# Kernel tuning notes

Measured on AMD Instinct MI355X. Metric: run time of the kernel, lower is better.

## Reference

```python
import jax, jax.numpy as jnp
import numpy as np

DIM = 96
HEADS = 3
HEAD_DIM = DIM // HEADS
WIN = (4, 4, 4)
N_WIN = WIN[0] * WIN[1] * WIN[2]  # 64 tokens per window
HIDDEN = int(DIM * 4.0)
EPS = 1e-5


def setup_inputs() -> dict:
    key = jax.random.key(0)
    ks = jax.random.split(key, 16)
    s = lambda fan: 1.0 / np.sqrt(fan)
    return {
        "x": jax.random.normal(ks[0], (1, 64, 96, 96, 96), jnp.float32),
        "g1": jnp.ones((DIM,), jnp.float32),
        "b1": jnp.zeros((DIM,), jnp.float32),
        "wq": jax.random.normal(ks[1], (DIM, DIM), jnp.float32) * s(DIM),
        "bq": jnp.zeros((DIM,), jnp.float32),
        "wkv": jax.random.normal(ks[2], (DIM, 2 * DIM), jnp.float32) * s(DIM),
        "bkv": jnp.zeros((2 * DIM,), jnp.float32),
        "wp": jax.random.normal(ks[3], (DIM, DIM), jnp.float32) * s(DIM),
        "bp": jnp.zeros((DIM,), jnp.float32),
        "g2": jnp.ones((DIM,), jnp.float32),
        "b2": jnp.zeros((DIM,), jnp.float32),
        "w1": jax.random.normal(ks[4], (DIM, HIDDEN), jnp.float32) * s(DIM),
        "bm1": jnp.zeros((HIDDEN,), jnp.float32),
        "w2": jax.random.normal(ks[5], (HIDDEN, DIM), jnp.float32) * s(HIDDEN),
        "bm2": jnp.zeros((DIM,), jnp.float32),
    }


def _layernorm(x, g, b):
    mu = jnp.mean(x, axis=-1, keepdims=True)
    var = jnp.mean(jnp.square(x - mu), axis=-1, keepdims=True)
    return (x - mu) * jax.lax.rsqrt(var + EPS) * g + b


def _window_partition(x):
    B, D, H, W, C = x.shape
    wd, wh, ww = WIN
    x = x.reshape(B, D // wd, wd, H // wh, wh, W // ww, ww, C)
    x = x.transpose(0, 1, 3, 5, 2, 4, 6, 7)
    return x.reshape(-1, N_WIN, C)


def _window_reverse(win, B, D, H, W):
    wd, wh, ww = WIN
    C = win.shape[-1]
    x = win.reshape(B, D // wd, H // wh, W // ww, wd, wh, ww, C)
    x = x.transpose(0, 1, 4, 2, 5, 3, 6, 7)
    return x.reshape(B, D, H, W, C)


def reference(x, g1, b1, wq, bq, wkv, bkv, wp, bp, g2, b2, w1, bm1, w2, bm2):
    B, D, H, W, C = x.shape
    # --- part 1: LN -> window attention -> residual ---
    h = _layernorm(x, g1, b1)
    # D,H,W chosen divisible by window size, so padding is a no-op
    xw = _window_partition(h)                       # (nW, N, C)
    nW = xw.shape[0]
    q = (xw @ wq + bq).reshape(nW, N_WIN, HEADS, HEAD_DIM)
    kv = (xw @ wkv + bkv).reshape(nW, N_WIN, 2, HEADS, HEAD_DIM)
    k, v = kv[:, :, 0], kv[:, :, 1]                 # (nW, N, h, hd)
    scale = HEAD_DIM ** -0.5
    attn = jnp.einsum("wnhd,wmhd->whnm", q * scale, k)
    attn = jax.nn.softmax(attn, axis=-1)
    out = jnp.einsum("whnm,wmhd->wnhd", attn, v).reshape(nW, N_WIN, C)
    out = out @ wp + bp
    attn_out = _window_reverse(out, B, D, H, W)
    x = x + attn_out
    # --- part 2: LN -> MLP -> residual ---
    h2 = _layernorm(x, g2, b2)
    h2 = jax.nn.gelu(h2 @ w1 + bm1, approximate=False) @ w2 + bm2
    return x + h2
```

## Files before the change

### kernel.cpp

```cpp
#include <hip/hip_runtime.h>

typedef __bf16 bf16x8 __attribute__((ext_vector_type(8)));
typedef __bf16 bf16x4 __attribute__((ext_vector_type(4)));
typedef float f32x4 __attribute__((ext_vector_type(4)));

#define MFMA(a,b,c) __builtin_amdgcn_mfma_f32_16x16x32_bf16(a, b, c, 0, 0, 0)

__device__ __forceinline__ float gelu_f(float t) {
    float t2 = t * t;
    float m = t * __builtin_fmaf(-0.07135481627f, t2, -1.5957691216f);
    float e = __expf(m);
    return t * __builtin_amdgcn_rcpf(1.0f + e);
}

__global__ void prep_weights(const float* __restrict__ wq, const float* __restrict__ wkv,
                             const float* __restrict__ wp, const float* __restrict__ w1,
                             const float* __restrict__ w2, __bf16* __restrict__ ws) {
    int i = blockIdx.x * 256 + threadIdx.x;
    const float scale = 0.17677669529663687f;
    if (i < 9216) {
        int n = i / 96, k = i % 96;
        ws[i] = (__bf16)(wq[k * 96 + n] * scale);
    } else if (i < 27648) {
        int j = i - 9216; int n = j / 96, k = j % 96;
        ws[i] = (__bf16)(wkv[k * 192 + n]);
    } else if (i < 36864) {
        int j = i - 27648; int n = j / 96, k = j % 96;
        ws[i] = (__bf16)(wp[k * 96 + n]);
    } else if (i < 73728) {
        int j = i - 36864; int n = j / 96, k = j % 96;
        ws[i] = (__bf16)(w1[k * 384 + n]);
    } else if (i < 110592) {
        int j = i - 73728; int n = j / 384, k = j % 384;
        ws[i] = (__bf16)(w2[k * 96 + n]);
    }
}

#define LDH 104

__global__ __launch_bounds__(256, 2) void attn_kernel(
    const float* __restrict__ x, const float* __restrict__ g1v, const float* __restrict__ b1v,
    const float* __restrict__ bq, const float* __restrict__ bkv, const float* __restrict__ bp,
    const __bf16* __restrict__ ws, float* __restrict__ xmid)
{
    const __bf16* wqt  = ws;
    const __bf16* wkvt = ws + 9216;
    const __bf16* wpt  = ws + 27648;

    __shared__ __align__(16) __bf16 h_lds[64 * LDH];
    __shared__ __align__(16) __bf16 q_lds[64 * LDH];
    __shared__ __align__(16) __bf16 k_lds[64 * LDH];
    __shared__ __align__(16) __bf16 vt_lds[96 * 72];
    __shared__ __align__(16) __bf16 p_lds[4 * 16 * 72];

    const int tid = threadIdx.x;
    const int wv = tid >> 6, lane = tid & 63;
    const int c = lane & 15, g = lane >> 4;
    const int mp = wv >> 1, ng = wv & 1;

    const int wid = blockIdx.x;
    const int wdI = wid / 576, rem = wid % 576, whI = rem / 24, wwI = rem % 24;
    const int tok = tid >> 2, cseg = (tid & 3) * 24;
    const int dz = tok >> 4, hy = (tok >> 2) & 3, wx = tok & 3;
    const long gbase = (((long)(wdI * 4 + dz) * 96 + (whI * 4 + hy)) * 96 + (wwI * 4 + wx)) * 96 + cseg;

    float xr[24];
    #pragma unroll
    for (int j = 0; j < 6; ++j) {
        float4 v = *reinterpret_cast<const float4*>(x + gbase + j * 4);
        xr[j*4+0] = v.x; xr[j*4+1] = v.y; xr[j*4+2] = v.z; xr[j*4+3] = v.w;
    }
    float s = 0.f;
    #pragma unroll
    for (int j = 0; j < 24; ++j) s += xr[j];
    s += __shfl_xor(s, 1); s += __shfl_xor(s, 2);
    float mu = s * (1.0f / 96.0f);
    float vs = 0.f;
    #pragma unroll
    for (int j = 0; j < 24; ++j) { float d = xr[j] - mu; vs += d * d; }
    vs += __shfl_xor(vs, 1); vs += __shfl_xor(vs, 2);
    float rstd = rsqrtf(vs * (1.0f / 96.0f) + 1e-5f);
    #pragma unroll
    for (int j = 0; j < 6; ++j) {
        float4 gv = *reinterpret_cast<const float4*>(g1v + cseg + j * 4);
        float4 bv = *reinterpret_cast<const float4*>(b1v + cseg + j * 4);
        h_lds[tok * LDH + cseg + j*4+0] = (__bf16)((xr[j*4+0] - mu) * rstd * gv.x + bv.x);
        h_lds[tok * LDH + cseg + j*4+1] = (__bf16)((xr[j*4+1] - mu) * rstd * gv.y + bv.y);
        h_lds[tok * LDH + cseg + j*4+2] = (__bf16)((xr[j*4+2] - mu) * rstd * gv.z + bv.z);
        h_lds[tok * LDH + cseg + j*4+3] = (__bf16)((xr[j*4+3] - mu) * rstd * gv.w + bv.w);
    }
    __syncthreads();

    {
        f32x4 acc[2][3];
        #pragma unroll
        for (int mi = 0; mi < 2; ++mi)
            #pragma unroll
            for (int nl = 0; nl < 3; ++nl) acc[mi][nl] = (f32x4){0.f, 0.f, 0.f, 0.f};
        #pragma unroll
        for (int kc = 0; kc < 3; ++kc) {
            bf16x8 a[2];
            #pragma unroll
            for (int mi = 0; mi < 2; ++mi)
                a[mi] = *reinterpret_cast<const bf16x8*>(&h_lds[((mp*2+mi)*16 + c) * LDH + kc*32 + g*8]);
            #pragma unroll
            for (int nl = 0; nl < 3; ++nl) {
                int nt = ng * 3 + nl;
                bf16x8 b = *reinterpret_cast<const bf16x8*>(&wqt[(nt*16 + c) * 96 + kc*32 + g*8]);
                #pragma unroll
                for (int mi = 0; mi < 2; ++mi)
                    acc[mi][nl] = MFMA(a[mi], b, acc[mi][nl]);
            }
        }
        #pragma unroll
        for (int nl = 0; nl < 3; ++nl) {
            int n = (ng * 3 + nl) * 16 + c;
            float bias = bq[n] * 0.17677669529663687f;
            #pragma unroll
            for (int mi = 0; mi < 2; ++mi)
                #pragma unroll
                for (int r = 0; r < 4; ++r)
                    q_lds[((mp*2+mi)*16 + g*4 + r) * LDH + n] = (__bf16)(acc[mi][nl][r] + bias);
        }
    }

    {
        f32x4 acc[4][3];
        #pragma unroll
        for (int m = 0; m < 4; ++m)
            #pragma unroll
            for (int nl = 0; nl < 3; ++nl) acc[m][nl] = (f32x4){0.f, 0.f, 0.f, 0.f};
        #pragma unroll
        for (int kc = 0; kc < 3; ++kc) {
            bf16x8 a[4];
            #pragma unroll
            for (int m = 0; m < 4; ++m)
                a[m] = *reinterpret_cast<const bf16x8*>(&h_lds[(m*16 + c) * LDH + kc*32 + g*8]);
            #pragma unroll
            for (int nl = 0; nl < 3; ++nl) {
                int nt = wv * 3 + nl;
                bf16x8 b = *reinterpret_cast<const bf16x8*>(&wkvt[(nt*16 + c) * 96 + kc*32 + g*8]);
                #pragma unroll
                for (int m = 0; m < 4; ++m)
                    acc[m][nl] = MFMA(a[m], b, acc[m][nl]);
            }
        }
        #pragma unroll
        for (int nl = 0; nl < 3; ++nl) {
            int n = (wv * 3 + nl) * 16 + c;
            float bias = bkv[n];
            if (wv < 2) {
                #pragma unroll
                for (int m = 0; m < 4; ++m)
                    #pragma unroll
                    for (int r = 0; r < 4; ++r)
                        k_lds[(m*16 + g*4 + r) * LDH + n] = (__bf16)(acc[m][nl][r] + bias);
            } else {
                int nv = n - 96;
                #pragma unroll
                for (int m = 0; m < 4; ++m) {
                    bf16x4 pk;
                    pk.x = (__bf16)(acc[m][nl][0] + bias);
                    pk.y = (__bf16)(acc[m][nl][1] + bias);
                    pk.z = (__bf16)(acc[m][nl][2] + bias);
                    pk.w = (__bf16)(acc[m][nl][3] + bias);
                    *reinterpret_cast<bf16x4*>(&vt_lds[nv * 72 + m*16 + g*4]) = pk;
                }
            }
        }
    }
    __syncthreads();

    __bf16* p_w = &p_lds[wv * (16 * 72)];
    #pragma unroll
    for (int h = 0; h < 3; ++h) {
        f32x4 sacc[4];
        #pragma unroll
        for (int nt = 0; nt < 4; ++nt) sacc[nt] = (f32x4){0.f, 0.f, 0.f, 0.f};
        bf16x8 a = *reinterpret_cast<const bf16x8*>(&q_lds[(wv*16 + c) * LDH + h*32 + g*8]);
        #pragma unroll
        for (int nt = 0; nt < 4; ++nt) {
            bf16x8 b = *reinterpret_cast<const bf16x8*>(&k_lds[(nt*16 + c) * LDH + h*32 + g*8]);
            sacc[nt] = MFMA(a, b, sacc[nt]);
        }
        float mx[4];
        #pragma unroll
        for (int r = 0; r < 4; ++r) {
            float m0 = fmaxf(fmaxf(sacc[0][r], sacc[1][r]), fmaxf(sacc[2][r], sacc[3][r]));
            m0 = fmaxf(m0, __shfl_xor(m0, 1));
            m0 = fmaxf(m0, __shfl_xor(m0, 2));
            m0 = fmaxf(m0, __shfl_xor(m0, 4));
            m0 = fmaxf(m0, __shfl_xor(m0, 8));
            mx[r] = m0;
        }
        float p[4][4];
        #pragma unroll
        for (int nt = 0; nt < 4; ++nt)
            #pragma unroll
            for (int r = 0; r < 4; ++r)
                p[nt][r] = __expf(sacc[nt][r] - mx[r]);
        float rsinv[4];
        #pragma unroll
        for (int r = 0; r < 4; ++r) {
            float s0 = p[0][r] + p[1][r] + p[2][r] + p[3][r];
            s0 += __shfl_xor(s0, 1); s0 += __shfl_xor(s0, 2);
            s0 += __shfl_xor(s0, 4); s0 += __shfl_xor(s0, 8);
            rsinv[r] = __builtin_amdgcn_rcpf(s0);
        }
        #pragma unroll
        for (int nt = 0; nt < 4; ++nt)
            #pragma unroll
            for (int r = 0; r < 4; ++r)
                p_w[(g*4 + r) * 72 + nt*16 + c] = (__bf16)p[nt][r];

        f32x4 oacc[2];
        oacc[0] = (f32x4){0.f, 0.f, 0.f, 0.f};
        oacc[1] = (f32x4){0.f, 0.f, 0.f, 0.f};
        #pragma unroll
        for (int kc = 0; kc < 2; ++kc) {
            bf16x8 pa = *reinterpret_cast<const bf16x8*>(&p_w[c * 72 + kc*32 + g*8]);
            #pragma unroll
            for (int n2 = 0; n2 < 2; ++n2) {
                bf16x8 b = *reinterpret_cast<const bf16x8*>(&vt_lds[(h*32 + n2*16 + c) * 72 + kc*32 + g*8]);
                oacc[n2] = MFMA(pa, b, oacc[n2]);
            }
        }
        #pragma unroll
        for (int n2 = 0; n2 < 2; ++n2)
            #pragma unroll
            for (int r = 0; r < 4; ++r)
                h_lds[(wv*16 + g*4 + r) * LDH + h*32 + n2*16 + c] = (__bf16)(oacc[n2][r] * rsinv[r]);
    }
    __syncthreads();

    {
        f32x4 acc[2][3];
        #pragma unroll
        for (int mi = 0; mi < 2; ++mi)
            #pragma unroll
            for (int nl = 0; nl < 3; ++nl) acc[mi][nl] = (f32x4){0.f, 0.f, 0.f, 0.f};
        #pragma unroll
        for (int kc = 0; kc < 3; ++kc) {
            bf16x8 a[2];
            #pragma unroll
            for (int mi = 0; mi < 2; ++mi)
                a[mi] = *reinterpret_cast<const bf16x8*>(&h_lds[((mp*2+mi)*16 + c) * LDH + kc*32 + g*8]);
            #pragma unroll
            for (int nl = 0; nl < 3; ++nl) {
                int nt = ng * 3 + nl;
                bf16x8 b = *reinterpret_cast<const bf16x8*>(&wpt[(nt*16 + c) * 96 + kc*32 + g*8]);
                #pragma unroll
                for (int mi = 0; mi < 2; ++mi)
                    acc[mi][nl] = MFMA(a[mi], b, acc[mi][nl]);
            }
        }
        __syncthreads();
        #pragma unroll
        for (int nl = 0; nl < 3; ++nl) {
            int n = (ng * 3 + nl) * 16 + c;
            float bias = bp[n];
            #pragma unroll
            for (int mi = 0; mi < 2; ++mi)
                #pragma unroll
                for (int r = 0; r < 4; ++r)
                    q_lds[((mp*2+mi)*16 + g*4 + r) * LDH + n] = (__bf16)(acc[mi][nl][r] + bias);
        }
    }
    __syncthreads();

    #pragma unroll
    for (int j = 0; j < 6; ++j) {
        float4 v;
        v.x = xr[j*4+0] + (float)q_lds[tok * LDH + cseg + j*4+0];
        v.y = xr[j*4+1] + (float)q_lds[tok * LDH + cseg + j*4+1];
        v.z = xr[j*4+2] + (float)q_lds[tok * LDH + cseg + j*4+2];
        v.w = xr[j*4+3] + (float)q_lds[tok * LDH + cseg + j*4+3];
        *reinterpret_cast<float4*>(xmid + gbase + j * 4) = v;
    }
}

#define LDU 104
#define LDC2 104

__global__ __launch_bounds__(384, 3) void mlp_kernel(
    float* __restrict__ xio, const float* __restrict__ g2v, const float* __restrict__ b2v,
    const float* __restrict__ bm1, const float* __restrict__ bm2,
    const __bf16* __restrict__ ws)
{
    const __bf16* w1t = ws + 36864;
    const __bf16* w2t = ws + 73728;

    __shared__ __align__(16) __bf16 u_lds[64 * LDU];
    __shared__ __align__(16) __bf16 hid[64 * LDC2];

    const int tid = threadIdx.x;
    const int wv = tid >> 6, lane = tid & 63;
    const int c = lane & 15, g = lane >> 4;

    const int tok = tid >> 2, cseg = (tid & 3) * 24;
    const long gaddr = ((long)blockIdx.x * 64 + tok) * 96 + cseg;

    const f32x4 fzero = {0.f, 0.f, 0.f, 0.f};

    if (tid < 256) {
        float xr[24];
        #pragma unroll
        for (int j = 0; j < 6; ++j) {
            float4 v = *reinterpret_cast<const float4*>(xio + gaddr + j * 4);
            xr[j*4+0] = v.x; xr[j*4+1] = v.y; xr[j*4+2] = v.z; xr[j*4+3] = v.w;
        }
        float s = 0.f;
        #pragma unroll
        for (int j = 0; j < 24; ++j) s += xr[j];
        s += __shfl_xor(s, 1); s += __shfl_xor(s, 2);
        float mu = s * (1.0f / 96.0f);
        float vs = 0.f;
        #pragma unroll
        for (int j = 0; j < 24; ++j) { float d = xr[j] - mu; vs += d * d; }
        vs += __shfl_xor(vs, 1); vs += __shfl_xor(vs, 2);
        float rstd = rsqrtf(vs * (1.0f / 96.0f) + 1e-5f);
        #pragma unroll
        for (int j = 0; j < 6; ++j) {
            f32x4 gv = *reinterpret_cast<const f32x4*>(g2v + cseg + j * 4);
            f32x4 bv = *reinterpret_cast<const f32x4*>(b2v + cseg + j * 4);
            bf16x4 o;
            #pragma unroll
            for (int r = 0; r < 4; ++r) o[r] = (__bf16)((xr[j*4+r] - mu) * rstd * gv[r] + bv[r]);
            *reinterpret_cast<bf16x4*>(&u_lds[tok * LDU + cseg + j*4]) = o;
        }
    }
    __syncthreads();

    bf16x8 bU[3][4];
    #pragma unroll
    for (int kc = 0; kc < 3; ++kc)
        #pragma unroll
        for (int tt = 0; tt < 4; ++tt)
            bU[kc][tt] = *reinterpret_cast<const bf16x8*>(&u_lds[(tt*16 + c) * LDU + kc*32 + g*8]);

    f32x4 accB[4];
    #pragma unroll
    for (int tt = 0; tt < 4; ++tt) accB[tt] = fzero;

    #pragma unroll
    for (int ch = 0; ch < 4; ++ch) {
        f32x4 accA[4];
        #pragma unroll
        for (int tt = 0; tt < 4; ++tt) accA[tt] = fzero;
        #pragma unroll
        for (int kc = 0; kc < 3; ++kc) {
            bf16x8 aW = *reinterpret_cast<const bf16x8*>(&w1t[((ch*6 + wv)*16 + c) * 96 + kc*32 + g*8]);
            #pragma unroll
            for (int tt = 0; tt < 4; ++tt)
                accA[tt] = MFMA(aW, bU[kc][tt], accA[tt]);
        }
        {
            f32x4 bb = *reinterpret_cast<const f32x4*>(&bm1[(ch*6 + wv)*16 + 4*g]);
            #pragma unroll
            for (int tt = 0; tt < 4; ++tt) {
                bf16x4 o;
                #pragma unroll
                for (int r = 0; r < 4; ++r) o[r] = (__bf16)gelu_f(accA[tt][r] + bb[r]);
                *reinterpret_cast<bf16x4*>(&hid[(tt*16 + c) * LDC2 + wv*16 + 4*g]) = o;
            }
        }
        __syncthreads();

        #pragma unroll
        for (int kc = 0; kc < 3; ++kc) {
            bf16x8 aW2 = *reinterpret_cast<const bf16x8*>(&w2t[(wv*16 + c) * 384 + ch*96 + kc*32 + g*8]);
            #pragma unroll
            for (int tt = 0; tt < 4; ++tt) {
                bf16x8 bHd = *reinterpret_cast<const bf16x8*>(&hid[(tt*16 + c) * LDC2 + kc*32 + g*8]);
                accB[tt] = MFMA(aW2, bHd, accB[tt]);
            }
        }
        if (ch < 3) __syncthreads();
    }

    {
        f32x4 bb = *reinterpret_cast<const f32x4*>(&bm2[wv*16 + 4*g]);
        #pragma unroll
        for (int tt = 0; tt < 4; ++tt) {
            bf16x4 o;
            #pragma unroll
            for (int r = 0; r < 4; ++r) o[r] = (__bf16)(accB[tt][r] + bb[r]);
            *reinterpret_cast<bf16x4*>(&u_lds[(tt*16 + c) * LDU + wv*16 + 4*g]) = o;
        }
    }
    __syncthreads();

    if (tid < 256) {
        #pragma unroll
        for (int j = 0; j < 6; ++j) {
            float4 xv = *reinterpret_cast<const float4*>(xio + gaddr + j * 4);
            bf16x4 mo = *reinterpret_cast<const bf16x4*>(&u_lds[tok * LDU + cseg + j*4]);
            float4 v;
            v.x = xv.x + (float)mo[0];
            v.y = xv.y + (float)mo[1];
            v.z = xv.z + (float)mo[2];
            v.w = xv.w + (float)mo[3];
            *reinterpret_cast<float4*>(xio + gaddr + j * 4) = v;
        }
    }
}

extern "C" void kernel_launch(void* const* d_in, const int* in_sizes, int n_in,
                              void* d_out, int out_size, void* d_ws, size_t ws_size,
                              hipStream_t stream) {
    (void)in_sizes; (void)n_in; (void)out_size; (void)ws_size;
    const float* x   = (const float*)d_in[0];
    const float* g1  = (const float*)d_in[1];
    const float* b1  = (const float*)d_in[2];
    const float* wq  = (const float*)d_in[3];
    const float* bq  = (const float*)d_in[4];
    const float* wkv = (const float*)d_in[5];
    const float* bkv = (const float*)d_in[6];
    const float* wp  = (const float*)d_in[7];
    const float* bp  = (const float*)d_in[8];
    const float* g2  = (const float*)d_in[9];
    const float* b2  = (const float*)d_in[10];
    const float* w1  = (const float*)d_in[11];
    const float* bm1 = (const float*)d_in[12];
    const float* w2  = (const float*)d_in[13];
    const float* bm2 = (const float*)d_in[14];
    float* out = (float*)d_out;
    __bf16* ws = (__bf16*)d_ws;

    prep_weights<<<432, 256, 0, stream>>>(wq, wkv, wp, w1, w2, ws);
    attn_kernel<<<9216, 256, 0, stream>>>(x, g1, b1, bq, bkv, bp, ws, out);
    mlp_kernel<<<9216, 384, 0, stream>>>(out, g2, b2, bm1, bm2, ws);
}
```

Baseline: 498.8 us.

## Restructure MLP kernel so each wave owns 16 tokens without block barriers

The MLP kernel moves from 6 waves that split hidden and output channels over all 64 tokens to 4 waves, each computing the full MLP for its own 16 tokens with private LDS scratch. This removes every __syncthreads and the idle threads during layernorm and residual. In exchange each wave now loads all W1/W2 weight fragments itself, which multiplies weight traffic from cache per block, and it holds 6 accumulators per stage instead of 4.

```diff
diff --git a/kernel.cpp b/kernel.cpp
--- a/kernel.cpp
+++ b/kernel.cpp
@@ -280,9 +280,8 @@
 }
 
 #define LDU 104
-#define LDC2 104
-
-__global__ __launch_bounds__(384, 3) void mlp_kernel(
+
+__global__ __launch_bounds__(256) void mlp_kernel(
     float* __restrict__ xio, const float* __restrict__ g2v, const float* __restrict__ b2v,
     const float* __restrict__ bm1, const float* __restrict__ bm2,
     const __bf16* __restrict__ ws)
@@ -290,19 +289,21 @@
     const __bf16* w1t = ws + 36864;
     const __bf16* w2t = ws + 73728;
 
-    __shared__ __align__(16) __bf16 u_lds[64 * LDU];
-    __shared__ __align__(16) __bf16 hid[64 * LDC2];
+    __shared__ __align__(16) __bf16 scr[4 * 2 * 16 * LDU];
 
     const int tid = threadIdx.x;
     const int wv = tid >> 6, lane = tid & 63;
     const int c = lane & 15, g = lane >> 4;
 
-    const int tok = tid >> 2, cseg = (tid & 3) * 24;
-    const long gaddr = ((long)blockIdx.x * 64 + tok) * 96 + cseg;
+    __bf16* uscr = scr + wv * (2 * 16 * LDU);
+    __bf16* hscr = uscr + 16 * LDU;
+
+    const int ltok = lane >> 2, cseg = (lane & 3) * 24;
+    const long gaddr = ((long)blockIdx.x * 64 + wv * 16 + ltok) * 96 + cseg;
 
     const f32x4 fzero = {0.f, 0.f, 0.f, 0.f};
 
-    if (tid < 256) {
+    {
         float xr[24];
         #pragma unroll
         for (int j = 0; j < 6; ++j) {
@@ -326,82 +327,70 @@
             bf16x4 o;
             #pragma unroll
             for (int r = 0; r < 4; ++r) o[r] = (__bf16)((xr[j*4+r] - mu) * rstd * gv[r] + bv[r]);
-            *reinterpret_cast<bf16x4*>(&u_lds[tok * LDU + cseg + j*4]) = o;
-        }
-    }
-    __syncthreads();
-
-    bf16x8 bU[3][4];
+            *reinterpret_cast<bf16x4*>(&uscr[ltok * LDU + cseg + j*4]) = o;
+        }
+    }
+
+    bf16x8 bU[3];
     #pragma unroll
     for (int kc = 0; kc < 3; ++kc)
-        #pragma unroll
-        for (int tt = 0; tt < 4; ++tt)
-            bU[kc][tt] = *reinterpret_cast<const bf16x8*>(&u_lds[(tt*16 + c) * LDU + kc*32 + g*8]);
-
-    f32x4 accB[4];
-    #pragma unroll
-    for (int tt = 0; tt < 4; ++tt) accB[tt] = fzero;
+        bU[kc] = *reinterpret_cast<const bf16x8*>(&uscr[c * LDU + kc*32 + g*8]);
+
+    f32x4 accB[6];
+    #pragma unroll
+    for (int nt = 0; nt < 6; ++nt) accB[nt] = fzero;
 
     #pragma unroll
     for (int ch = 0; ch < 4; ++ch) {
-        f32x4 accA[4];
-        #pragma unroll
-        for (int tt = 0; tt < 4; ++tt) accA[tt] = fzero;
+        f32x4 accA[6];
+        #pragma unroll
+        for (int nt = 0; nt < 6; ++nt) accA[nt] = fzero;
         #pragma unroll
         for (int kc = 0; kc < 3; ++kc) {
-            bf16x8 aW = *reinterpret_cast<const bf16x8*>(&w1t[((ch*6 + wv)*16 + c) * 96 + kc*32 + g*8]);
-            #pragma unroll
-            for (int tt = 0; tt < 4; ++tt)
-                accA[tt] = MFMA(aW, bU[kc][tt], accA[tt]);
-        }
-        {
-            f32x4 bb = *reinterpret_cast<const f32x4*>(&bm1[(ch*6 + wv)*16 + 4*g]);
-            #pragma unroll
-            for (int tt = 0; tt < 4; ++tt) {
-                bf16x4 o;
-                #pragma unroll
-                for (int r = 0; r < 4; ++r) o[r] = (__bf16)gelu_f(accA[tt][r] + bb[r]);
-                *reinterpret_cast<bf16x4*>(&hid[(tt*16 + c) * LDC2 + wv*16 + 4*g]) = o;
-            }
-        }
-        __syncthreads();
-
+            #pragma unroll
+            for (int nt = 0; nt < 6; ++nt) {
+                bf16x8 aW = *reinterpret_cast<const bf16x8*>(&w1t[((ch*6 + nt)*16 + c) * 96 + kc*32 + g*8]);
+                accA[nt] = MFMA(aW, bU[kc], accA[nt]);
+            }
+        }
+        #pragma unroll
+        for (int nt = 0; nt < 6; ++nt) {
+            f32x4 bb = *reinterpret_cast<const f32x4*>(&bm1[(ch*6 + nt)*16 + 4*g]);
+            bf16x4 o;
+            #pragma unroll
+            for (int r = 0; r < 4; ++r) o[r] = (__bf16)gelu_f(accA[nt][r] + bb[r]);
+            *reinterpret_cast<bf16x4*>(&hscr[c * LDU + nt*16 + 4*g]) = o;
+        }
         #pragma unroll
         for (int kc = 0; kc < 3; ++kc) {
-            bf16x8 aW2 = *reinterpret_cast<const bf16x8*>(&w2t[(wv*16 + c) * 384 + ch*96 + kc*32 + g*8]);
-            #pragma unroll
-            for (int tt = 0; tt < 4; ++tt) {
-                bf16x8 bHd = *reinterpret_cast<const bf16x8*>(&hid[(tt*16 + c) * LDC2 + kc*32 + g*8]);
-                accB[tt] = MFMA(aW2, bHd, accB[tt]);
-            }
-        }
-        if (ch < 3) __syncthreads();
-    }
-
-    {
-        f32x4 bb = *reinterpret_cast<const f32x4*>(&bm2[wv*16 + 4*g]);
-        #pragma unroll
-        for (int tt = 0; tt < 4; ++tt) {
-            bf16x4 o;
-            #pragma unroll
-            for (int r = 0; r < 4; ++r) o[r] = (__bf16)(accB[tt][r] + bb[r]);
-            *reinterpret_cast<bf16x4*>(&u_lds[(tt*16 + c) * LDU + wv*16 + 4*g]) = o;
-        }
-    }
-    __syncthreads();
-
-    if (tid < 256) {
-        #pragma unroll
-        for (int j = 0; j < 6; ++j) {
-            float4 xv = *reinterpret_cast<const float4*>(xio + gaddr + j * 4);
-            bf16x4 mo = *reinterpret_cast<const bf16x4*>(&u_lds[tok * LDU + cseg + j*4]);
-            float4 v;
-            v.x = xv.x + (float)mo[0];
-            v.y = xv.y + (float)mo[1];
-            v.z = xv.z + (float)mo[2];
-            v.w = xv.w + (float)mo[3];
-            *reinterpret_cast<float4*>(xio + gaddr + j * 4) = v;
-        }
+            bf16x8 bH = *reinterpret_cast<const bf16x8*>(&hscr[c * LDU + kc*32 + g*8]);
+            #pragma unroll
+            for (int nt = 0; nt < 6; ++nt) {
+                bf16x8 aW2 = *reinterpret_cast<const bf16x8*>(&w2t[(nt*16 + c) * 384 + ch*96 + kc*32 + g*8]);
+                accB[nt] = MFMA(aW2, bH, accB[nt]);
+            }
+        }
+    }
+
+    #pragma unroll
+    for (int nt = 0; nt < 6; ++nt) {
+        f32x4 bb = *reinterpret_cast<const f32x4*>(&bm2[nt*16 + 4*g]);
+        bf16x4 o;
+        #pragma unroll
+        for (int r = 0; r < 4; ++r) o[r] = (__bf16)(accB[nt][r] + bb[r]);
+        *reinterpret_cast<bf16x4*>(&uscr[c * LDU + nt*16 + 4*g]) = o;
+    }
+
+    #pragma unroll
+    for (int j = 0; j < 6; ++j) {
+        float4 xv = *reinterpret_cast<const float4*>(xio + gaddr + j * 4);
+        bf16x4 mo = *reinterpret_cast<const bf16x4*>(&uscr[ltok * LDU + cseg + j*4]);
+        float4 v;
+        v.x = xv.x + (float)mo[0];
+        v.y = xv.y + (float)mo[1];
+        v.z = xv.z + (float)mo[2];
+        v.w = xv.w + (float)mo[3];
+        *reinterpret_cast<float4*>(xio + gaddr + j * 4) = v;
     }
 }
 
@@ -429,5 +418,5 @@
 
     prep_weights<<<432, 256, 0, stream>>>(wq, wkv, wp, w1, w2, ws);
     attn_kernel<<<9216, 256, 0, stream>>>(x, g1, b1, bq, bkv, bp, ws, out);
-    mlp_kernel<<<9216, 384, 0, stream>>>(out, g2, b2, bm1, bm2, ws);
+    mlp_kernel<<<9216, 256, 0, stream>>>(out, g2, b2, bm1, bm2, ws);
 }
```

New measurement: 776.6 us. 55.7% more time.
